# Performance work log

Hardware: AMD Instinct MI355X
Metric: run time of the kernel (lower is better)

## Reference

```python
import jax, jax.numpy as jnp
import numpy as np

B, N, K = 8, 4096, 20
EC = (64, 64, 64, 128)


def setup_inputs() -> dict:
    key = jax.random.key(0)
    ks = jax.random.split(key, 12)
    d = {"points": jax.random.normal(ks[0], (B, 3, N), jnp.float32)}
    c_in = 3
    for i, c_out in enumerate(EC):
        d[f"ec_w{i}"] = jax.random.normal(ks[1 + i], (c_out, 2 * c_in), jnp.float32) * (1.0 / np.sqrt(2 * c_in))
        d[f"ec_s{i}"] = jnp.ones((c_out,), jnp.float32)
        d[f"ec_b{i}"] = jnp.zeros((c_out,), jnp.float32)
        c_in = c_out
    d["local_w"] = jax.random.normal(ks[5], (1024, 320), jnp.float32) * (1.0 / np.sqrt(320))
    d["local_s"] = jnp.ones((1024,), jnp.float32)
    d["local_b"] = jnp.zeros((1024,), jnp.float32)
    d["g_w0"] = jax.random.normal(ks[6], (512, 1024), jnp.float32) * (1.0 / np.sqrt(1024))
    d["g_s0"] = jnp.ones((512,), jnp.float32)
    d["g_b0"] = jnp.zeros((512,), jnp.float32)
    d["g_w1"] = jax.random.normal(ks[7], (256, 512), jnp.float32) * (1.0 / np.sqrt(512))
    d["g_s1"] = jnp.ones((256,), jnp.float32)
    d["g_b1"] = jnp.zeros((256,), jnp.float32)
    return d


def _knn_idx(pts):
    # pts: [B, 3, N]; squared euclidean pairwise distance, k nearest
    sq = jnp.sum(pts * pts, axis=1)  # [B, N]
    dist = sq[:, :, None] + sq[:, None, :] - 2.0 * jnp.einsum('bci,bcj->bij', pts, pts)  # [B, N, N]
    _, idx = jax.lax.top_k(-dist, K)  # [B, N, K] indices of k smallest distances
    return idx


def _edge_conv(x, idx, w, s, b):
    # x: [B, C, N], idx: [B, N, K]
    nb = jax.vmap(lambda xb, ib: xb[:, ib])(x, idx)  # gather neighbors -> [B, C, N, K]
    ctr = x[:, :, :, None]
    edge = jnp.concatenate([jnp.broadcast_to(ctr, nb.shape), nb - ctr], axis=1)  # [B, 2C, N, K]
    y = jnp.einsum('oc,bcnk->bonk', w, edge)  # 1x1 conv2d
    y = jax.nn.relu(s[None, :, None, None] * y + b[None, :, None, None])  # eval BN folded + ReLU
    return jnp.max(y, axis=3)  # max over neighbors -> [B, C_out, N]


def reference(points, ec_w0, ec_s0, ec_b0, ec_w1, ec_s1, ec_b1, ec_w2, ec_s2, ec_b2,
              ec_w3, ec_s3, ec_b3, local_w, local_s, local_b,
              g_w0, g_s0, g_b0, g_w1, g_s1, g_b1):
    idx = _knn_idx(points)  # computed once, reused (knn_ind=None path, feature_knn=False)
    x = points
    feats = []
    for w, s, b in ((ec_w0, ec_s0, ec_b0), (ec_w1, ec_s1, ec_b1),
                    (ec_w2, ec_s2, ec_b2), (ec_w3, ec_s3, ec_b3)):
        x = _edge_conv(x, idx, w, s, b)
        feats.append(x)
    cat = jnp.concatenate(feats, axis=1)  # [B, 320, N]
    loc = jax.nn.relu(local_s[None, :, None] * jnp.einsum('oc,bcn->bon', local_w, cat)
                      + local_b[None, :, None])  # [B, 1024, N]
    glob = jnp.max(loc, axis=2)            # [B, 1024]
    max_indices = jnp.argmax(loc, axis=2)  # [B, 1024]
    h = jax.nn.relu(g_s0 * (glob @ g_w0.T) + g_b0)   # [B, 512]
    out = jax.nn.relu(g_s1 * (h @ g_w1.T) + g_b1)    # [B, 256]
    return out, max_indices
```

## Files before the change

kernel.cpp:

```cpp
#include <hip/hip_runtime.h>
#include <hip/hip_bf16.h>

namespace {
constexpr int B = 8;
constexpr int N = 4096;
constexpr int KNN = 20;
constexpr int NSEG = 4;
constexpr int SEGLEN = N / NSEG;
constexpr int HSEG = SEGLEN / 2;
constexpr int CAP = 24;
constexpr int SLOTS = NSEG * CAP;

constexpr size_t OFF_IDX  = 0;
constexpr size_t SZ_IDX   = (size_t)B * N * KNN * 4;
constexpr size_t OFF_T    = OFF_IDX + SZ_IDX;
constexpr size_t SZ_T     = (size_t)B * N * 128 * 4;
constexpr size_t OFF_CAT  = OFF_T + SZ_T;
constexpr size_t SZ_CAT   = (size_t)B * N * 320 * 4;
constexpr size_t OFF_PV   = OFF_CAT + SZ_CAT;
constexpr size_t SZ_PV    = (size_t)B * 1024 * 32 * 4;
constexpr size_t OFF_PI   = OFF_PV + SZ_PV;
constexpr size_t OFF_GLOB = OFF_PI + SZ_PV;
constexpr size_t OFF_H    = OFF_GLOB + (size_t)B * 1024 * 4;
constexpr size_t OFF_LD   = OFF_T;
constexpr size_t SZ_LD    = (size_t)B * N * SLOTS * 4;
constexpr size_t OFF_LJ   = OFF_LD + SZ_LD;
constexpr size_t OFF_CNT  = OFF_LJ + SZ_LD;
}

typedef float v2f __attribute__((ext_vector_type(2)));

__device__ __forceinline__ float mulrn(float a, float b) {
#pragma clang fp contract(off)
  return a * b;
}
__device__ __forceinline__ float addrn(float a, float b) {
#pragma clang fp contract(off)
  return a + b;
}
__device__ __forceinline__ float subrn(float a, float b) {
#pragma clang fp contract(off)
  return a - b;
}
__device__ __forceinline__ v2f mulrn2(v2f a, v2f b) {
#pragma clang fp contract(off)
  return a * b;
}
__device__ __forceinline__ v2f addrn2(v2f a, v2f b) {
#pragma clang fp contract(off)
  return a + b;
}

__device__ __forceinline__ void pkmac_lo(v2f& acc, v2f w, v2f x) {
  v2f t;
  asm("v_pk_mul_f32 %1, %2, %3 op_sel:[0,0] op_sel_hi:[1,0]\n\t"
      "v_pk_add_f32 %0, %0, %1"
      : "+v"(acc), "=&v"(t) : "v"(w), "v"(x));
}
__device__ __forceinline__ void pkmac_hi(v2f& acc, v2f w, v2f x) {
  v2f t;
  asm("v_pk_mul_f32 %1, %2, %3 op_sel:[0,1] op_sel_hi:[1,1]\n\t"
      "v_pk_add_f32 %0, %0, %1"
      : "+v"(acc), "=&v"(t) : "v"(w), "v"(x));
}

__global__ __launch_bounds__(256) void knn_scan(
    const float* __restrict__ pts,
    float* __restrict__ listd, int* __restrict__ listj, int* __restrict__ counts) {
  __shared__ float4 sp[2 * SEGLEN];
  const int b = blockIdx.z;
  const int tid = threadIdx.x;
  const float* px = pts + (size_t)b * 3 * N;
  const int cb0 = blockIdx.y * 2 * SEGLEN;
  for (int i = tid; i < 2 * SEGLEN; i += 256) {
    const float x = px[cb0 + i];
    const float y = px[N + cb0 + i];
    const float z = px[2 * N + cb0 + i];
    const float sq = addrn(addrn(mulrn(x, x), mulrn(y, y)), mulrn(z, z));
    sp[i] = make_float4(x, y, z, sq);
  }
  __syncthreads();
  const int lane = tid & 63;
  const int rl = lane & 31;
  const int h2 = lane >> 5;
  const int segl = (tid >> 6) & 1;
  const int rg = tid >> 7;
  const int seg = blockIdx.y * 2 + segl;
  const int row0 = blockIdx.x * 128 + rg * 64 + rl;
  const int row1 = row0 + 32;
  const float ax = px[row0], ay = px[N + row0], az = px[2 * N + row0];
  const float bx = px[row1], by = px[N + row1], bz = px[2 * N + row1];
  const float4 qa = make_float4(ax, ay, az,
      addrn(addrn(mulrn(ax, ax), mulrn(ay, ay)), mulrn(az, az)));
  const float4 qb = make_float4(bx, by, bz,
      addrn(addrn(mulrn(bx, bx), mulrn(by, by)), mulrn(bz, bz)));
  float da[KNN], db[KNN];
#pragma unroll
  for (int t = 0; t < KNN; ++t) { da[t] = 3.0e38f; db[t] = 3.0e38f; }
  const int j0 = segl * SEGLEN + h2 * HSEG;
#pragma unroll 2
  for (int jj = 0; jj < HSEG; ++jj) {
    const float4 c = sp[j0 + jj];
    v2f t0 = mulrn2((v2f){qa.x, qb.x}, (v2f){c.x, c.x});
    t0 = addrn2(t0, mulrn2((v2f){qa.y, qb.y}, (v2f){c.y, c.y}));
    t0 = addrn2(t0, mulrn2((v2f){qa.z, qb.z}, (v2f){c.z, c.z}));
    v2f d2 = addrn2((v2f){qa.w, qb.w}, (v2f){c.w, c.w});
    d2 = d2 - mulrn2((v2f){2.0f, 2.0f}, t0);
    if (d2.x < da[KNN - 1]) {
      float cur = d2.x;
#pragma unroll
      for (int t = 0; t < KNN; ++t) {
        const float lo = fminf(cur, da[t]);
        cur = fmaxf(cur, da[t]);
        da[t] = lo;
      }
    }
    if (d2.y < db[KNN - 1]) {
      float cur = d2.y;
#pragma unroll
      for (int t = 0; t < KNN; ++t) {
        const float lo = fminf(cur, db[t]);
        cur = fmaxf(cur, db[t]);
        db[t] = lo;
      }
    }
  }
  float tha = -3.0e38f, thb = -3.0e38f;
#pragma unroll
  for (int i = 0; i < KNN; ++i) {
    tha = fmaxf(tha, fminf(da[i], __shfl_xor(da[KNN - 1 - i], 32)));
    thb = fmaxf(thb, fminf(db[i], __shfl_xor(db[KNN - 1 - i], 32)));
  }
  float* lda = listd + (size_t)(b * N + row0) * SLOTS + seg * CAP;
  int* lja = listj + (size_t)(b * N + row0) * SLOTS + seg * CAP;
  float* ldb = listd + (size_t)(b * N + row1) * SLOTS + seg * CAP;
  int* ljb = listj + (size_t)(b * N + row1) * SLOTS + seg * CAP;
  const int jg0 = cb0 + j0;
  int ca = 0, cb = 0;
#pragma unroll 2
  for (int jj = 0; jj < HSEG; ++jj) {
    const float4 c = sp[j0 + jj];
    v2f t0 = mulrn2((v2f){qa.x, qb.x}, (v2f){c.x, c.x});
    t0 = addrn2(t0, mulrn2((v2f){qa.y, qb.y}, (v2f){c.y, c.y}));
    t0 = addrn2(t0, mulrn2((v2f){qa.z, qb.z}, (v2f){c.z, c.z}));
    v2f d2 = addrn2((v2f){qa.w, qb.w}, (v2f){c.w, c.w});
    d2 = d2 - mulrn2((v2f){2.0f, 2.0f}, t0);
    if (d2.x <= tha && ca < CAP) {
      const int sl = h2 ? (CAP - 1 - ca) : ca;
      lda[sl] = d2.x; lja[sl] = jg0 + jj; ++ca;
    }
    if (d2.y <= thb && cb < CAP) {
      const int sl = h2 ? (CAP - 1 - cb) : cb;
      ldb[sl] = d2.y; ljb[sl] = jg0 + jj; ++cb;
    }
  }
  const int oa = __shfl_xor(ca, 32);
  const int ob = __shfl_xor(cb, 32);
  if (h2 == 0) {
    counts[(b * N + row0) * NSEG + seg] = ca | (oa << 16);
    counts[(b * N + row1) * NSEG + seg] = cb | (ob << 16);
  }
}

__global__ __launch_bounds__(256) void knn_merge(
    const float* __restrict__ listd, const int* __restrict__ listj,
    const int* __restrict__ counts, int* __restrict__ idxout) {
  __shared__ unsigned long long keys[64][SLOTS + 1];
  const int r0 = blockIdx.x * 64;
  const int t = threadIdx.x;
  for (int i = t; i < 64 * SLOTS; i += 256) {
    const int rr = i / SLOTS;
    const int sl = i % SLOTS;
    const int seg = sl / CAP;
    const int e = sl % CAP;
    const int row = r0 + rr;
    unsigned long long key = 0xFFFFFFFE00000000ULL | (unsigned)row;
    const int cp = counts[row * NSEG + seg];
    if (e < (cp & 0xFFFF) || e >= CAP - (cp >> 16)) {
      const float d = listd[(size_t)row * SLOTS + sl];
      unsigned ub = __float_as_uint(d);
      ub ^= (ub & 0x80000000u) ? 0xFFFFFFFFu : 0x80000000u;
      key = ((unsigned long long)ub << 32) | (unsigned)listj[(size_t)row * SLOTS + sl];
    }
    keys[rr][sl] = key;
  }
  __syncthreads();
  const int g4 = t & 3;
  const int rr = t >> 2;
  const int sbase = g4 * 24;
  int* outp = idxout + (size_t)(r0 + rr) * KNN;
  for (int sel = 0; sel < KNN; ++sel) {
    unsigned long long best = ~0ULL;
    int bs = sbase;
#pragma unroll
    for (int e = 0; e < 24; ++e) {
      const unsigned long long k2 = keys[rr][sbase + e];
      if (k2 < best) { best = k2; bs = sbase + e; }
    }
    unsigned long long m = best;
    {
      const unsigned long long o1 = __shfl_xor(m, 1);
      m = (o1 < m) ? o1 : m;
      const unsigned long long o2 = __shfl_xor(m, 2);
      m = (o2 < m) ? o2 : m;
    }
    if (best == m) keys[rr][bs] = ~0ULL;
    if (g4 == 0) outp[sel] = (int)(m & 0xFFFFFFFFu);
  }
}


__global__ __launch_bounds__(256) void ec_layer1(
    const float* __restrict__ pts, const int* __restrict__ idx,
    const float* __restrict__ w, const float* __restrict__ s,
    const float* __restrict__ bi, float* __restrict__ cat) {
  const int b = blockIdx.y;
  const int n = blockIdx.x * 4 + (threadIdx.x >> 6);
  const int o = threadIdx.x & 63;
  const float* p = pts + (size_t)b * 3 * N;
  const float xix = p[n], xiy = p[N + n], xiz = p[2 * N + n];
  const float* wr = w + o * 6;
  const float w0 = wr[0], w1 = wr[1], w2 = wr[2], w3 = wr[3], w4 = wr[4], w5 = wr[5];
  float P = mulrn(w0, xix);
  P = addrn(P, mulrn(w1, xiy));
  P = addrn(P, mulrn(w2, xiz));
  const float so = s[o], bo = bi[o];
  const int* ip = idx + ((size_t)b * N + n) * KNN;
  float m = 0.0f;
#pragma unroll 4
  for (int k = 0; k < KNN; ++k) {
    int j = ip[k];
    if ((unsigned)j >= (unsigned)N) j = n;
    const float ex = subrn(p[j], xix);
    const float ey = subrn(p[N + j], xiy);
    const float ez = subrn(p[2 * N + j], xiz);
    float acc = addrn(P, mulrn(w3, ex));
    acc = addrn(acc, mulrn(w4, ey));
    acc = addrn(acc, mulrn(w5, ez));
    m = fmaxf(m, addrn(mulrn(so, acc), bo));
  }
  cat[((size_t)b * N + n) * 320 + o] = m;
}

template <int OH>
__global__ __launch_bounds__(256) void ec_edge(
    const float* __restrict__ cat, int inoff, const int* __restrict__ idx,
    const float* __restrict__ w, const float* __restrict__ s,
    const float* __restrict__ bi, float* __restrict__ catout, int outoff) {
  constexpr int EST = 164;
  constexpr int RS = 68;
  constexpr int PS = 64 * OH + 4;
  constexpr int WS = 64 * OH + 4;
  __shared__ float U[80 * RS];
  __shared__ float xis[8][64];
  __shared__ float Pt[8 * PS];
  __shared__ float Wl2[16 * WS];
  __shared__ int jl[160];
  const int t = threadIdx.x;
  const int b = blockIdx.y;
  const int n0 = blockIdx.x * 8;
  const size_t bN = (size_t)b * N;

#pragma unroll
  for (int q = 0; q < 2; ++q) {
    const int p = (t >> 6) + 4 * q;
    const int c = t & 63;
    xis[p][c] = cat[(bN + n0 + p) * 320 + inoff + c];
  }
  if (t < 160) {
    const int p = t / 20;
    const int k = t % 20;
    int j = idx[(bN + n0 + p) * KNN + k];
    if ((unsigned)j >= (unsigned)N) j = n0 + p;
    jl[t] = j;
  }
  __syncthreads();

#pragma unroll
  for (int ho = 0; ho < OH; ++ho) {
#pragma unroll
    for (int q = 0; q < 16; ++q) {
      const int l = t + 256 * q;
      U[(l >> 6) * 66 + (l & 63)] = w[(ho * 64 + (l >> 6)) * 128 + (l & 63)];
    }
    __syncthreads();
    {
      const int o = t & 63;
      const int p0 = t >> 6;
      const float2* wq = (const float2*)&U[o * 66];
      const float2* x0 = (const float2*)&xis[p0][0];
      const float2* x1 = (const float2*)&xis[p0 + 4][0];
      float2 wv = wq[0];
      float2 a0 = x0[0];
      float2 a1 = x1[0];
      float P0 = mulrn(wv.x, a0.x);
      float P1 = mulrn(wv.x, a1.x);
      P0 = addrn(P0, mulrn(wv.y, a0.y));
      P1 = addrn(P1, mulrn(wv.y, a1.y));
#pragma unroll
      for (int c2 = 1; c2 < 32; ++c2) {
        wv = wq[c2];
        a0 = x0[c2];
        a1 = x1[c2];
        P0 = addrn(P0, mulrn(wv.x, a0.x));
        P1 = addrn(P1, mulrn(wv.x, a1.x));
        P0 = addrn(P0, mulrn(wv.y, a0.y));
        P1 = addrn(P1, mulrn(wv.y, a1.y));
      }
      Pt[p0 * PS + ho * 64 + o] = P0;
      Pt[(p0 + 4) * PS + ho * 64 + o] = P1;
    }
    __syncthreads();
  }

  const int g = t & 15;
  const int h = t >> 4;
  v2f a4[2][4][2 * OH];
  v2f a2p[2][2 * OH];
#pragma unroll
  for (int i = 0; i < 2; ++i) {
    const int p = (64 * i + 4 * g) / 20;
#pragma unroll
    for (int ho = 0; ho < OH; ++ho) {
      const float4 Pv = *(const float4*)&Pt[p * PS + ho * 64 + 4 * h];
#pragma unroll
      for (int e = 0; e < 4; ++e) {
        a4[i][e][2 * ho] = (v2f){Pv.x, Pv.y};
        a4[i][e][2 * ho + 1] = (v2f){Pv.z, Pv.w};
      }
    }
  }
  {
    const int p = (128 + 2 * g) / 20;
#pragma unroll
    for (int ho = 0; ho < OH; ++ho) {
      const float4 Pv = *(const float4*)&Pt[p * PS + ho * 64 + 4 * h];
#pragma unroll
      for (int e = 0; e < 2; ++e) {
        a2p[e][2 * ho] = (v2f){Pv.x, Pv.y};
        a2p[e][2 * ho + 1] = (v2f){Pv.z, Pv.w};
      }
    }
  }

  for (int kc = 0; kc < 64; kc += 16) {
#pragma unroll
    for (int ho = 0; ho < OH; ++ho) {
      const int o = t >> 2;
      const int cq = t & 3;
      const float4 wv = *(const float4*)&w[(ho * 64 + o) * 128 + 64 + kc + 4 * cq];
      Wl2[(4 * cq + 0) * WS + ho * 64 + o] = wv.x;
      Wl2[(4 * cq + 1) * WS + ho * 64 + o] = wv.y;
      Wl2[(4 * cq + 2) * WS + ho * 64 + o] = wv.z;
      Wl2[(4 * cq + 3) * WS + ho * 64 + o] = wv.w;
    }
#pragma unroll
    for (int q = 0; q < 3; ++q) {
      const int sl = 64 * q + (t >> 2);
      const int cq = t & 3;
      if (sl < 160) {
        const int p = sl / 20;
        const int j = jl[sl];
        const float4 xj = *(const float4*)&cat[(bN + j) * 320 + inoff + kc + 4 * cq];
        const float4 xv = *(const float4*)&xis[p][kc + 4 * cq];
        U[(4 * cq + 0) * EST + sl] = subrn(xj.x, xv.x);
        U[(4 * cq + 1) * EST + sl] = subrn(xj.y, xv.y);
        U[(4 * cq + 2) * EST + sl] = subrn(xj.z, xv.z);
        U[(4 * cq + 3) * EST + sl] = subrn(xj.w, xv.w);
      }
    }
    __syncthreads();
#pragma unroll
    for (int k = 0; k < 16; ++k) {
      const v2f e0lo = *(const v2f*)&U[k * EST + 4 * g];
      const v2f e0hi = *(const v2f*)&U[k * EST + 4 * g + 2];
      const v2f e1lo = *(const v2f*)&U[k * EST + 64 + 4 * g];
      const v2f e1hi = *(const v2f*)&U[k * EST + 64 + 4 * g + 2];
      const v2f e2 = *(const v2f*)&U[k * EST + 128 + 2 * g];
#pragma unroll
      for (int ho = 0; ho < OH; ++ho) {
        const v2f w01 = *(const v2f*)&Wl2[k * WS + ho * 64 + 4 * h];
        const v2f w23 = *(const v2f*)&Wl2[k * WS + ho * 64 + 4 * h + 2];
        pkmac_lo(a4[0][0][2 * ho], w01, e0lo);
        pkmac_lo(a4[0][0][2 * ho + 1], w23, e0lo);
        pkmac_hi(a4[0][1][2 * ho], w01, e0lo);
        pkmac_hi(a4[0][1][2 * ho + 1], w23, e0lo);
        pkmac_lo(a4[0][2][2 * ho], w01, e0hi);
        pkmac_lo(a4[0][2][2 * ho + 1], w23, e0hi);
        pkmac_hi(a4[0][3][2 * ho], w01, e0hi);
        pkmac_hi(a4[0][3][2 * ho + 1], w23, e0hi);
        pkmac_lo(a4[1][0][2 * ho], w01, e1lo);
        pkmac_lo(a4[1][0][2 * ho + 1], w23, e1lo);
        pkmac_hi(a4[1][1][2 * ho], w01, e1lo);
        pkmac_hi(a4[1][1][2 * ho + 1], w23, e1lo);
        pkmac_lo(a4[1][2][2 * ho], w01, e1hi);
        pkmac_lo(a4[1][2][2 * ho + 1], w23, e1hi);
        pkmac_hi(a4[1][3][2 * ho], w01, e1hi);
        pkmac_hi(a4[1][3][2 * ho + 1], w23, e1hi);
        pkmac_lo(a2p[0][2 * ho], w01, e2);
        pkmac_lo(a2p[0][2 * ho + 1], w23, e2);
        pkmac_hi(a2p[1][2 * ho], w01, e2);
        pkmac_hi(a2p[1][2 * ho + 1], w23, e2);
      }
    }
    __syncthreads();
  }

#pragma unroll
  for (int ho = 0; ho < OH; ++ho) {
    const float4 sv = *(const float4*)&s[ho * 64 + 4 * h];
    const float4 bv = *(const float4*)&bi[ho * 64 + 4 * h];
    const float sc[4] = {sv.x, sv.y, sv.z, sv.w};
    const float bc[4] = {bv.x, bv.y, bv.z, bv.w};
#pragma unroll
    for (int i = 0; i < 2; ++i) {
#pragma unroll
      for (int ep = 0; ep < 2; ++ep) {
        const int row = 32 * i + 2 * g + ep;
        float gm[4] = {0.f, 0.f, 0.f, 0.f};
#pragma unroll
        for (int ee = 0; ee < 2; ++ee) {
          const int e = 2 * ep + ee;
#pragma unroll
          for (int u = 0; u < 4; ++u) {
            const v2f a = a4[i][e][2 * ho + (u >> 1)];
            const float av = (u & 1) ? a.y : a.x;
            gm[u] = fmaxf(gm[u], fmaxf(addrn(mulrn(sc[u], av), bc[u]), 0.f));
          }
        }
        *(float4*)&U[row * RS + 4 * h] = make_float4(gm[0], gm[1], gm[2], gm[3]);
      }
    }
    {
      const int row = 64 + g;
      float gm[4] = {0.f, 0.f, 0.f, 0.f};
#pragma unroll
      for (int e = 0; e < 2; ++e) {
#pragma unroll
        for (int u = 0; u < 4; ++u) {
          const v2f a = a2p[e][2 * ho + (u >> 1)];
          const float av = (u & 1) ? a.y : a.x;
          gm[u] = fmaxf(gm[u], fmaxf(addrn(mulrn(sc[u], av), bc[u]), 0.f));
        }
      }
      *(float4*)&U[row * RS + 4 * h] = make_float4(gm[0], gm[1], gm[2], gm[3]);
    }
    __syncthreads();
#pragma unroll
    for (int q = 0; q < 2; ++q) {
      const int o = t & 63;
      const int p = (t >> 6) + 4 * q;
      const float* ur = &U[(10 * p) * RS + o];
      float m = ur[0];
#pragma unroll
      for (int r = 1; r < 10; ++r) m = fmaxf(m, ur[r * RS]);
      catout[(bN + n0 + p) * 320 + outoff + ho * 64 + o] = m;
    }
    if (ho + 1 < OH) __syncthreads();
  }
}

__global__ __launch_bounds__(256) void local_gemm(
    const float* __restrict__ cat, const float* __restrict__ w,
    const float* __restrict__ s, const float* __restrict__ bi,
    float* __restrict__ pval, int* __restrict__ pidx) {
  constexpr int KC = 16;
  constexpr int XS = 132;
  constexpr int BUF = KC * XS * 2;
  __shared__ float smem[2 * BUF];
  const int t = threadIdx.x;
  const int q0 = blockIdx.y * 128;
  const int ptile = blockIdx.x;
  const size_t pt0 = (size_t)ptile * 128;
  const int g = t & 15;
  const int h = t >> 4;
  v2f acc2[2][2][4][2];
#pragma unroll
  for (int ep = 0; ep < 2; ++ep)
#pragma unroll
    for (int fp = 0; fp < 2; ++fp)
#pragma unroll
      for (int pi = 0; pi < 4; ++pi)
#pragma unroll
        for (int u = 0; u < 2; ++u) acc2[ep][fp][pi][u] = (v2f){0.f, 0.f};

  const int lk = t & 15;
  const int lp = t >> 4;
  const int px = ((lk >> 3) & 1) << 1;
  const float* catp = cat + pt0 * 320 + lk;
  const float* wp = w + (size_t)q0 * 320 + lk;
  float rx[8], rw[8];
#pragma unroll
  for (int i = 0; i < 8; ++i) rx[i] = catp[(size_t)(lp + 16 * i) * 320];
#pragma unroll
  for (int i = 0; i < 8; ++i) rw[i] = wp[(size_t)(lp + 16 * i) * 320];
  {
    float* xs0 = smem;
    float* ws0 = smem + KC * XS;
#pragma unroll
    for (int i = 0; i < 8; ++i) xs0[lk * XS + ((lp + 16 * i) ^ px)] = rx[i];
#pragma unroll
    for (int i = 0; i < 8; ++i) ws0[lk * XS + ((lp + 16 * i) ^ px)] = rw[i];
  }

#pragma unroll 2
  for (int ch = 0; ch < 20; ++ch) {
    const int par = ch & 1;
    const float* xsr = smem + par * BUF;
    const float* wsr = xsr + KC * XS;
    if (ch + 1 < 20) {
      const int ko = (ch + 1) * KC;
#pragma unroll
      for (int i = 0; i < 8; ++i) rx[i] = catp[(size_t)(lp + 16 * i) * 320 + ko];
#pragma unroll
      for (int i = 0; i < 8; ++i) rw[i] = wp[(size_t)(lp + 16 * i) * 320 + ko];
    }
    __syncthreads();
#pragma unroll
    for (int k = 0; k < KC; ++k) {
      const int pm2 = ((k >> 3) & 1) << 1;
      const float* wrow = &wsr[k * XS];
      const float* xrow = &xsr[k * XS];
      v2f wA[2], wB[2];
#pragma unroll
      for (int fp = 0; fp < 2; ++fp) {
        wA[fp] = *(const v2f*)&wrow[64 * fp + 4 * h + pm2];
        wB[fp] = *(const v2f*)&wrow[64 * fp + 4 * h + (2 - pm2)];
      }
#pragma unroll
      for (int ep = 0; ep < 2; ++ep) {
        const v2f xq0 = *(const v2f*)&xrow[64 * ep + 4 * g + pm2];
        const v2f xq1 = *(const v2f*)&xrow[64 * ep + 4 * g + (2 - pm2)];
#pragma unroll
        for (int fp = 0; fp < 2; ++fp) {
          pkmac_lo(acc2[ep][fp][0][0], wA[fp], xq0);
          pkmac_lo(acc2[ep][fp][0][1], wB[fp], xq0);
          pkmac_hi(acc2[ep][fp][1][0], wA[fp], xq0);
          pkmac_hi(acc2[ep][fp][1][1], wB[fp], xq0);
          pkmac_lo(acc2[ep][fp][2][0], wA[fp], xq1);
          pkmac_lo(acc2[ep][fp][2][1], wB[fp], xq1);
          pkmac_hi(acc2[ep][fp][3][0], wA[fp], xq1);
          pkmac_hi(acc2[ep][fp][3][1], wB[fp], xq1);
        }
      }
    }
    if (ch + 1 < 20) {
      float* xsw = smem + (par ^ 1) * BUF;
      float* wsw = xsw + KC * XS;
#pragma unroll
      for (int i = 0; i < 8; ++i) xsw[lk * XS + ((lp + 16 * i) ^ px)] = rx[i];
#pragma unroll
      for (int i = 0; i < 8; ++i) wsw[lk * XS + ((lp + 16 * i) ^ px)] = rw[i];
    }
  }
  const int bb = ptile >> 5;
  const int blk = ptile & 31;
  float mv[8];
  int mi[8];
#pragma unroll
  for (int fp = 0; fp < 2; ++fp)
#pragma unroll
    for (int c = 0; c < 4; ++c) {
      const int f = fp * 4 + c;
      const int cl = 64 * fp + 4 * h + c;
      const float sc = s[q0 + cl];
      const float bc = bi[q0 + cl];
      mv[f] = -1.f;
      mi[f] = 0;
#pragma unroll
      for (int ep = 0; ep < 2; ++ep)
#pragma unroll
        for (int pi = 0; pi < 4; ++pi) {
          const v2f a2 = acc2[ep][fp][pi][c >> 1];
          const float a = (c & 1) ? a2.y : a2.x;
          const float v = fmaxf(addrn(mulrn(sc, a), bc), 0.f);
          if (v > mv[f]) { mv[f] = v; mi[f] = 64 * ep + 4 * g + pi; }
        }
    }
  __syncthreads();
  float* smv = smem;
  int* smi = (int*)(smem + 16 * 132);
#pragma unroll
  for (int fp = 0; fp < 2; ++fp)
#pragma unroll
    for (int c = 0; c < 4; ++c) {
      const int cl = 64 * fp + 4 * h + c;
      smv[g * 132 + cl] = mv[fp * 4 + c];
      smi[g * 132 + cl] = mi[fp * 4 + c];
    }
  __syncthreads();
  if (t < 128) {
    float best = smv[t];
    int bidx = smi[t];
    for (int gg = 1; gg < 16; ++gg) {
      const float v = smv[gg * 132 + t];
      const int vi = smi[gg * 132 + t];
      if (v > best || (v == best && vi < bidx)) { best = v; bidx = vi; }
    }
    const int n_l = blk * 128 + bidx;
    const size_t po = ((size_t)bb * 1024 + q0 + t) * 32 + blk;
    pval[po] = best;
    pidx[po] = n_l;
  }
}

__global__ __launch_bounds__(256) void final_reduce(
    const float* __restrict__ pval, const int* __restrict__ pidx,
    float* __restrict__ glob, float* __restrict__ oidx) {
  const int o = blockIdx.x * 256 + threadIdx.x;
  const float* pv = pval + (size_t)o * 32;
  const int* pi = pidx + (size_t)o * 32;
  float best = pv[0];
  int bi = pi[0];
  for (int k = 1; k < 32; ++k) {
    const float v = pv[k];
    if (v > best) { best = v; bi = pi[k]; }
  }
  glob[o] = best;
  oidx[o] = (float)bi;
}

template <int KIN, int OUTS>
__global__ __launch_bounds__(256) void dense_wave(
    const float* __restrict__ in, const float* __restrict__ w,
    const float* __restrict__ s, const float* __restrict__ bi,
    float* __restrict__ out) {
  const int wid = (blockIdx.x * 256 + threadIdx.x) >> 6;
  const int lane = threadIdx.x & 63;
  const int b = wid / OUTS;
  const int o = wid % OUTS;
  const float* ip = in + (size_t)b * KIN;
  const float* wr = w + (size_t)o * KIN;
  float acc = 0.f;
  for (int k = lane; k < KIN; k += 64) acc = fmaf(wr[k], ip[k], acc);
#pragma unroll
  for (int off = 32; off; off >>= 1) acc += __shfl_down(acc, off);
  if (lane == 0) out[(size_t)b * OUTS + o] = fmaxf(fmaf(s[o], acc, bi[o]), 0.f);
}

extern "C" void kernel_launch(void* const* d_in, const int* in_sizes, int n_in,
                              void* d_out, int out_size, void* d_ws, size_t ws_size,
                              hipStream_t stream) {
  (void)in_sizes; (void)n_in; (void)out_size; (void)ws_size;
  const float* pts = (const float*)d_in[0];
  const float* ec_w[4] = {(const float*)d_in[1], (const float*)d_in[4],
                          (const float*)d_in[7], (const float*)d_in[10]};
  const float* ec_s[4] = {(const float*)d_in[2], (const float*)d_in[5],
                          (const float*)d_in[8], (const float*)d_in[11]};
  const float* ec_b[4] = {(const float*)d_in[3], (const float*)d_in[6],
                          (const float*)d_in[9], (const float*)d_in[12]};
  const float* local_w = (const float*)d_in[13];
  const float* local_s = (const float*)d_in[14];
  const float* local_b = (const float*)d_in[15];
  const float* g_w0 = (const float*)d_in[16];
  const float* g_s0 = (const float*)d_in[17];
  const float* g_b0 = (const float*)d_in[18];
  const float* g_w1 = (const float*)d_in[19];
  const float* g_s1 = (const float*)d_in[20];
  const float* g_b1 = (const float*)d_in[21];

  char* ws = (char*)d_ws;
  int* idxbuf = (int*)(ws + OFF_IDX);
  float* cat = (float*)(ws + OFF_CAT);
  float* pv = (float*)(ws + OFF_PV);
  int* pi = (int*)(ws + OFF_PI);
  float* glob = (float*)(ws + OFF_GLOB);
  float* hbuf = (float*)(ws + OFF_H);
  float* listd = (float*)(ws + OFF_LD);
  int* listj = (int*)(ws + OFF_LJ);
  int* counts = (int*)(ws + OFF_CNT);
  float* outv = (float*)d_out;
  float* oidx = outv + 2048;

  knn_scan<<<dim3(32, 2, 8), 256, 0, stream>>>(pts, listd, listj, counts);
  knn_merge<<<dim3(512), 256, 0, stream>>>(listd, listj, counts, idxbuf);

  ec_layer1<<<dim3(1024, 8), 256, 0, stream>>>(pts, idxbuf, ec_w[0], ec_s[0], ec_b[0], cat);
  ec_edge<1><<<dim3(512, 8), 256, 0, stream>>>(cat, 0, idxbuf, ec_w[1], ec_s[1], ec_b[1], cat, 64);
  ec_edge<1><<<dim3(512, 8), 256, 0, stream>>>(cat, 64, idxbuf, ec_w[2], ec_s[2], ec_b[2], cat, 128);
  ec_edge<2><<<dim3(512, 8), 256, 0, stream>>>(cat, 128, idxbuf, ec_w[3], ec_s[3], ec_b[3], cat, 192);

  local_gemm<<<dim3(256, 8), 256, 0, stream>>>(cat, local_w, local_s, local_b, pv, pi);
  final_reduce<<<dim3(32), 256, 0, stream>>>(pv, pi, glob, oidx);
  dense_wave<1024, 512><<<dim3(1024), 256, 0, stream>>>(glob, g_w0, g_s0, g_b0, hbuf);
  dense_wave<512, 256><<<dim3(512), 256, 0, stream>>>(hbuf, g_w1, g_s1, g_b1, outv);
}
```

Measured before the change: 1.314 ms.

## Scan one row per thread in knn_scan and double block count across segments

The kNN scan kernel now handles one query row per thread instead of two packed rows. Each block covers a single segment rather than two, and the grid doubles along y to keep coverage the same. The aim is to cut register pressure from the two 20-entry sorted lists and to reduce divergence from the two independent insertion branches, which should raise occupancy and parallelism. In exchange it gives up the packed-math v2f distance computation and loads each candidate point from LDS once per row instead of once per two rows.

```diff
diff --git a/kernel.cpp b/kernel.cpp
--- a/kernel.cpp
+++ b/kernel.cpp
@@ -67,12 +67,13 @@
 __global__ __launch_bounds__(256) void knn_scan(
     const float* __restrict__ pts,
     float* __restrict__ listd, int* __restrict__ listj, int* __restrict__ counts) {
-  __shared__ float4 sp[2 * SEGLEN];
+  __shared__ float4 sp[SEGLEN];
   const int b = blockIdx.z;
   const int tid = threadIdx.x;
   const float* px = pts + (size_t)b * 3 * N;
-  const int cb0 = blockIdx.y * 2 * SEGLEN;
-  for (int i = tid; i < 2 * SEGLEN; i += 256) {
+  const int seg = blockIdx.y;
+  const int cb0 = seg * SEGLEN;
+  for (int i = tid; i < SEGLEN; i += 256) {
     const float x = px[cb0 + i];
     const float y = px[N + cb0 + i];
     const float z = px[2 * N + cb0 + i];
@@ -83,31 +84,23 @@
   const int lane = tid & 63;
   const int rl = lane & 31;
   const int h2 = lane >> 5;
-  const int segl = (tid >> 6) & 1;
-  const int rg = tid >> 7;
-  const int seg = blockIdx.y * 2 + segl;
-  const int row0 = blockIdx.x * 128 + rg * 64 + rl;
-  const int row1 = row0 + 32;
-  const float ax = px[row0], ay = px[N + row0], az = px[2 * N + row0];
-  const float bx = px[row1], by = px[N + row1], bz = px[2 * N + row1];
-  const float4 qa = make_float4(ax, ay, az,
-      addrn(addrn(mulrn(ax, ax), mulrn(ay, ay)), mulrn(az, az)));
-  const float4 qb = make_float4(bx, by, bz,
-      addrn(addrn(mulrn(bx, bx), mulrn(by, by)), mulrn(bz, bz)));
-  float da[KNN], db[KNN];
-#pragma unroll
-  for (int t = 0; t < KNN; ++t) { da[t] = 3.0e38f; db[t] = 3.0e38f; }
-  const int j0 = segl * SEGLEN + h2 * HSEG;
+  const int wid = tid >> 6;
+  const int row = blockIdx.x * 128 + wid * 32 + rl;
+  const float ax = px[row], ay = px[N + row], az = px[2 * N + row];
+  const float qw = addrn(addrn(mulrn(ax, ax), mulrn(ay, ay)), mulrn(az, az));
+  float da[KNN];
+#pragma unroll
+  for (int t = 0; t < KNN; ++t) da[t] = 3.0e38f;
+  const int j0 = h2 * HSEG;
 #pragma unroll 2
   for (int jj = 0; jj < HSEG; ++jj) {
     const float4 c = sp[j0 + jj];
-    v2f t0 = mulrn2((v2f){qa.x, qb.x}, (v2f){c.x, c.x});
-    t0 = addrn2(t0, mulrn2((v2f){qa.y, qb.y}, (v2f){c.y, c.y}));
-    t0 = addrn2(t0, mulrn2((v2f){qa.z, qb.z}, (v2f){c.z, c.z}));
-    v2f d2 = addrn2((v2f){qa.w, qb.w}, (v2f){c.w, c.w});
-    d2 = d2 - mulrn2((v2f){2.0f, 2.0f}, t0);
-    if (d2.x < da[KNN - 1]) {
-      float cur = d2.x;
+    float t0 = mulrn(ax, c.x);
+    t0 = addrn(t0, mulrn(ay, c.y));
+    t0 = addrn(t0, mulrn(az, c.z));
+    const float d2 = subrn(addrn(qw, c.w), mulrn(2.0f, t0));
+    if (d2 < da[KNN - 1]) {
+      float cur = d2;
 #pragma unroll
       for (int t = 0; t < KNN; ++t) {
         const float lo = fminf(cur, da[t]);
@@ -115,51 +108,32 @@
         da[t] = lo;
       }
     }
-    if (d2.y < db[KNN - 1]) {
-      float cur = d2.y;
-#pragma unroll
-      for (int t = 0; t < KNN; ++t) {
-        const float lo = fminf(cur, db[t]);
-        cur = fmaxf(cur, db[t]);
-        db[t] = lo;
-      }
-    }
-  }
-  float tha = -3.0e38f, thb = -3.0e38f;
-#pragma unroll
-  for (int i = 0; i < KNN; ++i) {
+  }
+  float tha = -3.0e38f;
+#pragma unroll
+  for (int i = 0; i < KNN; ++i)
     tha = fmaxf(tha, fminf(da[i], __shfl_xor(da[KNN - 1 - i], 32)));
-    thb = fmaxf(thb, fminf(db[i], __shfl_xor(db[KNN - 1 - i], 32)));
-  }
-  float* lda = listd + (size_t)(b * N + row0) * SLOTS + seg * CAP;
-  int* lja = listj + (size_t)(b * N + row0) * SLOTS + seg * CAP;
-  float* ldb = listd + (size_t)(b * N + row1) * SLOTS + seg * CAP;
-  int* ljb = listj + (size_t)(b * N + row1) * SLOTS + seg * CAP;
+  float* lda = listd + (size_t)(b * N + row) * SLOTS + seg * CAP;
+  int* lja = listj + (size_t)(b * N + row) * SLOTS + seg * CAP;
   const int jg0 = cb0 + j0;
-  int ca = 0, cb = 0;
+  int ca = 0;
 #pragma unroll 2
   for (int jj = 0; jj < HSEG; ++jj) {
     const float4 c = sp[j0 + jj];
-    v2f t0 = mulrn2((v2f){qa.x, qb.x}, (v2f){c.x, c.x});
-    t0 = addrn2(t0, mulrn2((v2f){qa.y, qb.y}, (v2f){c.y, c.y}));
-    t0 = addrn2(t0, mulrn2((v2f){qa.z, qb.z}, (v2f){c.z, c.z}));
-    v2f d2 = addrn2((v2f){qa.w, qb.w}, (v2f){c.w, c.w});
-    d2 = d2 - mulrn2((v2f){2.0f, 2.0f}, t0);
-    if (d2.x <= tha && ca < CAP) {
+    float t0 = mulrn(ax, c.x);
+    t0 = addrn(t0, mulrn(ay, c.y));
+    t0 = addrn(t0, mulrn(az, c.z));
+    const float d2 = subrn(addrn(qw, c.w), mulrn(2.0f, t0));
+    if (d2 <= tha && ca < CAP) {
       const int sl = h2 ? (CAP - 1 - ca) : ca;
-      lda[sl] = d2.x; lja[sl] = jg0 + jj; ++ca;
-    }
-    if (d2.y <= thb && cb < CAP) {
-      const int sl = h2 ? (CAP - 1 - cb) : cb;
-      ldb[sl] = d2.y; ljb[sl] = jg0 + jj; ++cb;
+      lda[sl] = d2;
+      lja[sl] = jg0 + jj;
+      ++ca;
     }
   }
   const int oa = __shfl_xor(ca, 32);
-  const int ob = __shfl_xor(cb, 32);
-  if (h2 == 0) {
-    counts[(b * N + row0) * NSEG + seg] = ca | (oa << 16);
-    counts[(b * N + row1) * NSEG + seg] = cb | (ob << 16);
-  }
+  if (h2 == 0)
+    counts[(b * N + row) * NSEG + seg] = ca | (oa << 16);
 }
 
 __global__ __launch_bounds__(256) void knn_merge(
@@ -672,7 +646,7 @@
   float* outv = (float*)d_out;
   float* oidx = outv + 2048;
 
-  knn_scan<<<dim3(32, 2, 8), 256, 0, stream>>>(pts, listd, listj, counts);
+  knn_scan<<<dim3(32, 4, 8), 256, 0, stream>>>(pts, listd, listj, counts);
   knn_merge<<<dim3(512), 256, 0, stream>>>(listd, listj, counts, idxbuf);
 
   ec_layer1<<<dim3(1024, 8), 256, 0, stream>>>(pts, idxbuf, ec_w[0], ec_s[0], ec_b[0], cat);
```

New measurement: 1.263 ms. 1.04x faster.
